# Optimization experiments

Hardware: AMD Instinct MI355X
Metric: run time of the kernel (lower is better)

The kernel has to match this reference:

```python
import jax, jax.numpy as jnp
import numpy as np

V, T, E, HID = 32000, 48, 128, 256
B, L = 256, 512
H = HID // 2  # per-direction LSTM hidden


def setup_inputs() -> dict:
    key = jax.random.key(0)
    ks = jax.random.split(key, 16)
    lengths = jax.random.randint(ks[0], (B,), L // 2, L + 1)
    mask = (jnp.arange(L)[None, :] < lengths[:, None])  # (B, L) bool, step 0 always on
    words = jax.random.randint(ks[1], (B, L), 1, V).astype(jnp.int32)
    words = jnp.where(mask, words, 0)  # padding_idx = 0
    tags = jax.random.randint(ks[2], (B, L), 0, T).astype(jnp.int32)
    s = 0.1
    emb = jax.random.normal(ks[3], (V, E), jnp.float32) * s
    emb = emb.at[0].set(0.0)  # padding_idx row zeroed
    Wih_f = jax.random.normal(ks[4], (4 * H, E), jnp.float32) * s
    Whh_f = jax.random.normal(ks[5], (4 * H, H), jnp.float32) * s
    bih_f = jax.random.normal(ks[6], (4 * H,), jnp.float32) * s
    bhh_f = jax.random.normal(ks[7], (4 * H,), jnp.float32) * s
    Wih_b = jax.random.normal(ks[8], (4 * H, E), jnp.float32) * s
    Whh_b = jax.random.normal(ks[9], (4 * H, H), jnp.float32) * s
    bih_b = jax.random.normal(ks[10], (4 * H,), jnp.float32) * s
    bhh_b = jax.random.normal(ks[11], (4 * H,), jnp.float32) * s
    Wout = jax.random.normal(ks[12], (T, HID), jnp.float32) * s
    bout = jax.random.normal(ks[13], (T,), jnp.float32) * s
    trans = jax.random.normal(ks[14], (T, T), jnp.float32) * s
    se = jax.random.normal(ks[15], (2, T), jnp.float32) * s
    return dict(words=words, tags=tags, mask=mask, emb=emb,
                Wih_f=Wih_f, Whh_f=Whh_f, bih_f=bih_f, bhh_f=bhh_f,
                Wih_b=Wih_b, Whh_b=Whh_b, bih_b=bih_b, bhh_b=bhh_b,
                Wout=Wout, bout=bout, trans=trans,
                start_trans=se[0], end_trans=se[1])


def _lstm_dir(x, Wih, Whh, bih, bhh, reverse):
    # x: (L, B, E) -> hs: (L, B, H); PyTorch gate order i, f, g, o
    Lx, Bx, _ = x.shape
    Hx = Whh.shape[1]
    def step(carry, xt):
        h, c = carry
        g = xt @ Wih.T + h @ Whh.T + (bih + bhh)
        i, f, gg, o = jnp.split(g, 4, axis=-1)
        c = jax.nn.sigmoid(f) * c + jax.nn.sigmoid(i) * jnp.tanh(gg)
        h = jax.nn.sigmoid(o) * jnp.tanh(c)
        return (h, c), h
    init = (jnp.zeros((Bx, Hx), x.dtype), jnp.zeros((Bx, Hx), x.dtype))
    _, hs = jax.lax.scan(step, init, x, reverse=reverse)
    return hs


def reference(words, tags, mask, emb, Wih_f, Whh_f, bih_f, bhh_f,
              Wih_b, Whh_b, bih_b, bhh_b, Wout, bout, trans,
              start_trans, end_trans):
    Bn = words.shape[0]
    # --- features: embedding -> BiLSTM -> linear ---
    x = emb[words].transpose(1, 0, 2)          # (L, B, E)
    h_f = _lstm_dir(x, Wih_f, Whh_f, bih_f, bhh_f, reverse=False)
    h_b = _lstm_dir(x, Wih_b, Whh_b, bih_b, bhh_b, reverse=True)
    h = jnp.concatenate([h_f, h_b], axis=-1)   # (L, B, 2H)
    emis = h @ Wout.T + bout                   # (L, B, T)
    mT = mask.T                                # (L, B) bool
    mF = mT.astype(emis.dtype)
    tT = tags.T.astype(jnp.int32)              # (L, B)

    # --- CRF numerator: score of gold path ---
    barange = jnp.arange(Bn)
    num0 = start_trans[tT[0]] + emis[0, barange, tT[0]]
    def num_step(score, inp):
        em_t, tag_prev, tag_t, m_t = inp
        step_score = trans[tag_prev, tag_t] + em_t[barange, tag_t]
        return score + step_score * m_t, None
    num, _ = jax.lax.scan(num_step, num0, (emis[1:], tT[:-1], tT[1:], mF[1:]))
    seq_ends = mF.sum(0).astype(jnp.int32) - 1
    last_tags = tT[seq_ends, barange]
    num = num + end_trans[last_tags]

    # --- CRF denominator: forward algorithm (logsumexp recurrence) ---
    den0 = start_trans[None, :] + emis[0]      # (B, T)
    def den_step(score, inp):
        em_t, m_t = inp
        nxt = jax.nn.logsumexp(score[:, :, None] + trans[None] + em_t[:, None, :], axis=1)
        return jnp.where(m_t[:, None], nxt, score), None
    den, _ = jax.lax.scan(den_step, den0, (emis[1:], mT[1:]))
    denom = jax.nn.logsumexp(den + end_trans[None, :], axis=1)

    llh = num - denom
    return -llh.mean()  # reduction='mean', negated
```

## Files before the change

### kernel.cpp

```cpp
#include <hip/hip_runtime.h>
#include <hip/hip_bf16.h>

typedef unsigned short ushort_t;
typedef unsigned int uint_t;
typedef __bf16 bf16x8 __attribute__((ext_vector_type(8)));
typedef float f32x4 __attribute__((ext_vector_type(4)));

#define L2E 1.44269504088896340736f
#define LN2 0.69314718055994530942f

#define WGBAR() __asm__ volatile("s_waitcnt lgkmcnt(0)\n\ts_barrier" ::: "memory")

static __device__ __forceinline__ float fexp2(float x) { return __builtin_amdgcn_exp2f(x); }
static __device__ __forceinline__ float flog2(float x) { return __builtin_amdgcn_logf(x); }
static __device__ __forceinline__ float frcp (float x) { return __builtin_amdgcn_rcpf(x); }

static __device__ __forceinline__ float sigm(float x) {
  return frcp(1.0f + fexp2(-L2E * x));
}
static __device__ __forceinline__ float tanha(float x) {
  return 1.0f - 2.0f * frcp(1.0f + fexp2(2.0f * L2E * x));
}

static __device__ __forceinline__ uint_t cvtpk(float lo, float hi) {
  uint_t r;
  asm("v_cvt_pk_bf16_f32 %0, %1, %2" : "=v"(r) : "v"(lo), "v"(hi));
  return r;
}
static __device__ __forceinline__ bf16x8 pack8(float4 a, float4 b) {
  uint4 u = make_uint4(cvtpk(a.x, a.y), cvtpk(a.z, a.w),
                       cvtpk(b.x, b.y), cvtpk(b.z, b.w));
  return __builtin_bit_cast(bf16x8, u);
}
static __device__ __forceinline__ uint2 pack4(float4 a) {
  return make_uint2(cvtpk(a.x, a.y), cvtpk(a.z, a.w));
}

template <int K>
static __device__ __forceinline__ float rotk(float x) {
  if constexpr (K == 0) {
    return x;
  } else {
    return __builtin_bit_cast(float, __builtin_amdgcn_update_dpp(
        0, __builtin_bit_cast(int, x), 0x120 + K, 0xf, 0xf, true));
  }
}

__global__ __launch_bounds__(512, 2) void k2_lstm(
    const int* __restrict__ words, const float* __restrict__ emb,
    const float* __restrict__ Wih_f, const float* __restrict__ Whh_f,
    const float* __restrict__ bih_f, const float* __restrict__ bhh_f,
    const float* __restrict__ Wih_b, const float* __restrict__ Whh_b,
    const float* __restrict__ bih_b, const float* __restrict__ bhh_b,
    ushort_t* __restrict__ hT, float* __restrict__ loss_out) {
  const int wg = blockIdx.x;
  const int dir = wg >> 7;
  const int r0 = (wg & 127) << 1;
  if (wg == 0 && threadIdx.x == 0) loss_out[0] = 0.f;
  const float* Whh = dir ? Whh_b : Whh_f;
  const float* Wih = dir ? Wih_b : Wih_f;
  const float* bih = dir ? bih_b : bih_f;
  const float* bhh = dir ? bhh_b : bhh_f;

  const int tid = threadIdx.x;
  const int w = tid >> 6;
  const int lane = tid & 63;
  const int l15 = lane & 15;
  const int kq = lane >> 4;

  __shared__ __align__(16) ushort_t hx[2][2][136];
  __shared__ __align__(16) ushort_t xp[2][16][128][4];
  __shared__ __align__(16) ushort_t xs[2][16][136];

  bf16x8 wfh[4][4], wfx[4][4];
  float biasP[4];
#pragma unroll
  for (int Q = 0; Q < 4; ++Q) {
    const int n = Q * 128 + w * 16 + l15;
    biasP[Q] = bih[n] + bhh[n];
#pragma unroll
    for (int c = 0; c < 4; ++c) {
      const int k0 = c * 32 + kq * 8;
      const float* sh = Whh + n * 128 + k0;
      const float* sx = Wih + n * 128 + k0;
      wfh[Q][c] = pack8(*(const float4*)sh, *(const float4*)(sh + 4));
      wfx[Q][c] = pack8(*(const float4*)sx, *(const float4*)(sx + 4));
    }
  }

  const int ur = (lane >> 4) & 1;
  const int uj = w * 16 + l15;
  float cst = 0.f;
  const f32x4 fz = {0.f, 0.f, 0.f, 0.f};

  const int sm = tid >> 5;
  const int sc = (tid & 31) * 4;
  const int str = r0 + (sm & 1);
  const int stl = sm >> 1;

  uint_t pd0[4], pd1[4];
  f32x4 pc = {0.f, 0.f, 0.f, 0.f};
  f32x4 pcsv = {0.f, 0.f, 0.f, 0.f};

  if (tid < 256) hx[0][tid >> 7][tid & 127] = 0;
  {
    const int tg = stl;
    const int tf = dir ? (511 - tg) : tg;
    const int word = words[str * 512 + tf];
    float4 av = *(const float4*)(emb + (size_t)word * 128 + sc);
    *(uint2*)&xs[1][sm][sc] = pack4(av);
  }
  WGBAR();
  {
    f32x4 qv[4];
#pragma unroll
    for (int Q = 0; Q < 4; ++Q) {
      f32x4 pc0 = {biasP[Q], biasP[Q], biasP[Q], biasP[Q]};
#pragma unroll
      for (int c = 0; c < 4; ++c) {
        bf16x8 af = __builtin_bit_cast(bf16x8, *(const uint4*)&xs[1][l15][kq * 8 + c * 32]);
        pc0 = __builtin_amdgcn_mfma_f32_16x16x32_bf16(af, wfx[Q][c], pc0, 0, 0, 0);
      }
      qv[Q] = pc0;
    }
#pragma unroll
    for (int rr = 0; rr < 4; ++rr) {
      pd0[rr] = cvtpk(qv[0][rr], qv[1][rr]);
      pd1[rr] = cvtpk(qv[2][rr], qv[3][rr]);
      *(uint2*)&xp[0][kq * 4 + rr][uj][0] = make_uint2(pd0[rr], pd1[rr]);
    }
  }
  {
    const int tg = 8 + stl;
    const int tf = dir ? (511 - tg) : tg;
    const int word = words[str * 512 + tf];
    float4 av = *(const float4*)(emb + (size_t)word * 128 + sc);
    *(uint2*)&xs[0][sm][sc] = pack4(av);
  }
  WGBAR();

  int sword = 0;
  float4 se0 = make_float4(0.f, 0.f, 0.f, 0.f);

#pragma unroll 1
  for (int i = 0; i < 64; ++i) {
    const int pcon = i & 1;
    const int ppro = pcon ^ 1;
    bf16x8 afp[4];
    if (i < 63) {
#pragma unroll
      for (int c = 0; c < 4; ++c)
        afp[c] = __builtin_bit_cast(bf16x8, *(const uint4*)&xs[pcon][l15][kq * 8 + c * 32]);
    }
#pragma unroll
    for (int s = 0; s < 8; ++s) {
      const int t = i * 8 + s;
      const int p = t & 1;
      const uint2 xq = *(const uint2*)&xp[pcon][2 * s + ur][uj][0];
      if (i < 62) {
        if (s == 0) {
          const int tg = (i + 2) * 8 + stl;
          const int tf = dir ? (511 - tg) : tg;
          sword = words[str * 512 + tf];
        }
        if (s == 2) se0 = *(const float4*)(emb + (size_t)sword * 128 + sc);
        if (s == 6) *(uint2*)&xs[ppro][sm][sc] = pack4(se0);
      }
      f32x4 a0, a1, a2, a3;
      const ushort_t* abase = &hx[p][l15 & 1][kq * 8];
      {
        bf16x8 af = __builtin_bit_cast(bf16x8, *(const uint4*)(abase));
        a0 = __builtin_amdgcn_mfma_f32_16x16x32_bf16(af, wfh[0][0], fz, 0, 0, 0);
        a1 = __builtin_amdgcn_mfma_f32_16x16x32_bf16(af, wfh[1][0], fz, 0, 0, 0);
        a2 = __builtin_amdgcn_mfma_f32_16x16x32_bf16(af, wfh[2][0], fz, 0, 0, 0);
        a3 = __builtin_amdgcn_mfma_f32_16x16x32_bf16(af, wfh[3][0], fz, 0, 0, 0);
      }
#pragma unroll
      for (int c = 1; c < 4; ++c) {
        bf16x8 af = __builtin_bit_cast(bf16x8, *(const uint4*)(abase + c * 32));
        a0 = __builtin_amdgcn_mfma_f32_16x16x32_bf16(af, wfh[0][c], a0, 0, 0, 0);
        a1 = __builtin_amdgcn_mfma_f32_16x16x32_bf16(af, wfh[1][c], a1, 0, 0, 0);
        a2 = __builtin_amdgcn_mfma_f32_16x16x32_bf16(af, wfh[2][c], a2, 0, 0, 0);
        a3 = __builtin_amdgcn_mfma_f32_16x16x32_bf16(af, wfh[3][c], a3, 0, 0, 0);
      }
      if (i < 63) {
        const int Q = s >> 1;
        if ((s & 1) == 0) {
          pc = f32x4{biasP[Q], biasP[Q], biasP[Q], biasP[Q]};
          pc = __builtin_amdgcn_mfma_f32_16x16x32_bf16(afp[0], wfx[Q][0], pc, 0, 0, 0);
          pc = __builtin_amdgcn_mfma_f32_16x16x32_bf16(afp[1], wfx[Q][1], pc, 0, 0, 0);
        } else {
          pc = __builtin_amdgcn_mfma_f32_16x16x32_bf16(afp[2], wfx[Q][2], pc, 0, 0, 0);
          pc = __builtin_amdgcn_mfma_f32_16x16x32_bf16(afp[3], wfx[Q][3], pc, 0, 0, 0);
          if ((s & 2) == 0) {
            pcsv = pc;
          } else if (s == 3) {
#pragma unroll
            for (int rr = 0; rr < 4; ++rr) pd0[rr] = cvtpk(pcsv[rr], pc[rr]);
          } else {
#pragma unroll
            for (int rr = 0; rr < 4; ++rr) {
              pd1[rr] = cvtpk(pcsv[rr], pc[rr]);
              *(uint2*)&xp[ppro][kq * 4 + rr][uj][0] = make_uint2(pd0[rr], pd1[rr]);
            }
          }
        }
      }
      const float g0 = (ur ? a0[1] : a0[0]) + __builtin_bit_cast(float, xq.x << 16);
      const float g1 = (ur ? a1[1] : a1[0]) + __builtin_bit_cast(float, xq.x & 0xffff0000u);
      const float g2 = (ur ? a2[1] : a2[0]) + __builtin_bit_cast(float, xq.y << 16);
      const float g3 = (ur ? a3[1] : a3[0]) + __builtin_bit_cast(float, xq.y & 0xffff0000u);
      const float si = sigm(g0), sf = sigm(g1), so = sigm(g3);
      const float tg = tanha(g2);
      cst = sf * cst + si * tg;
      const float h = so * tanha(cst);
      const ushort_t hb = (ushort_t)cvtpk(h, h);
      if (lane < 32) {
        hx[p ^ 1][ur][uj] = hb;
        const int tf = dir ? (511 - t) : t;
        hT[((size_t)(r0 + ur) * 512 + tf) * 256 + (dir << 7) + uj] = hb;
      }
      WGBAR();
    }
  }
}

#define K4_ROW(OP, m) \
  OP(m, 0) OP(m, 1) OP(m, 2) OP(m, 3) OP(m, 4) OP(m, 5) OP(m, 6) OP(m, 7) \
  OP(m, 8) OP(m, 9) OP(m, 10) OP(m, 11) OP(m, 12) OP(m, 13) OP(m, 14) OP(m, 15)
#define K4_ALL(OP) K4_ROW(OP, 0) K4_ROW(OP, 1) K4_ROW(OP, 2) K4_ROW(OP, 3)

#define ROTMOD_0  ""
#define ROTMOD_1  "row_ror:1 row_mask:0xf bank_mask:0xf"
#define ROTMOD_2  "row_ror:2 row_mask:0xf bank_mask:0xf"
#define ROTMOD_3  "row_ror:3 row_mask:0xf bank_mask:0xf"
#define ROTMOD_4  "row_ror:4 row_mask:0xf bank_mask:0xf"
#define ROTMOD_5  "row_ror:5 row_mask:0xf bank_mask:0xf"
#define ROTMOD_6  "row_ror:6 row_mask:0xf bank_mask:0xf"
#define ROTMOD_7  "row_ror:7 row_mask:0xf bank_mask:0xf"
#define ROTMOD_8  "row_ror:8 row_mask:0xf bank_mask:0xf"
#define ROTMOD_9  "row_ror:9 row_mask:0xf bank_mask:0xf"
#define ROTMOD_10 "row_ror:10 row_mask:0xf bank_mask:0xf"
#define ROTMOD_11 "row_ror:11 row_mask:0xf bank_mask:0xf"
#define ROTMOD_12 "row_ror:12 row_mask:0xf bank_mask:0xf"
#define ROTMOD_13 "row_ror:13 row_mask:0xf bank_mask:0xf"
#define ROTMOD_14 "row_ror:14 row_mask:0xf bank_mask:0xf"
#define ROTMOD_15 "row_ror:15 row_mask:0xf bank_mask:0xf"

#define K4_FMA(m_, k_) asm( \
    "v_fmac_f32 %0, %1, %2 " ROTMOD_##k_ \
    : "+v"(acc[((m_) * 16 + (k_)) & 7]) \
    : "v"(dm[m_]), "v"(pcr[(m_) * 16 + (k_)]));

#define K4_BODY(FOLD, LOADSTMT, ENSRC, MBIT, MEAS)                            \
  {                                                                           \
    float E = Ecur;                                                           \
    int eApp = 0;                                                             \
    if (FOLD) {                                                               \
      const float sc_ =                                                       \
          __builtin_bit_cast(float, (uint_t)(127 - e_pend) << 23);            \
      E *= sc_;                                                               \
      eApp = e_pend;                                                          \
    }                                                                         \
    LOADSTMT;                                                                 \
    const float En = fexp2((ENSRC) * L2E);                                    \
    float dm[4];                                                              \
    dm[0] = d;                                                                \
    dm[1] = __shfl_xor(d, 16, 64);                                            \
    dm[2] = __shfl_xor(d, 32, 64);                                            \
    dm[3] = __shfl_xor(d, 48, 64);                                            \
    float acc[8] = {0.f, 0.f, 0.f, 0.f, 0.f, 0.f, 0.f, 0.f};                  \
    K4_ALL(K4_FMA)                                                            \
    const float nxt = (((acc[0] + acc[1]) + (acc[2] + acc[3])) +              \
                       ((acc[4] + acc[5]) + (acc[6] + acc[7]))) * E;          \
    if (MBIT) {                                                               \
      d = v ? nxt : 0.f;                                                      \
      S += eApp;                                                              \
    }                                                                         \
    if (MEAS) {                                                               \
      const int db_ =                                                         \
          __builtin_amdgcn_readfirstlane(__builtin_bit_cast(int, d));         \
      e_pend = ((db_ >> 23) & 0xff) - 127;                                    \
    }                                                                         \
    Ecur = En;                                                                \
  }

#define EMLDS(tt) emis_t[((tt) >> 6) & 1][(tt) & 63][jj]

__global__ __launch_bounds__(128, 1) void k4_fused(
    const int* __restrict__ words, const int* __restrict__ tags,
    const ushort_t* __restrict__ hT, const float* __restrict__ Wout,
    const float* __restrict__ bout, const float* __restrict__ trans,
    const float* __restrict__ st, const float* __restrict__ et,
    float* __restrict__ out) {
  const int b = blockIdx.x;
  const int tid = threadIdx.x;
  const int wv = tid >> 6;
  const int lane = tid & 63;
  const int l15 = lane & 15;
  const int kq = lane >> 4;

  __shared__ __align__(16) ushort_t wfrag[3][8][64][8];
  __shared__ float emis_t[2][64][50];
  __shared__ float res[2];

  const ushort_t* hb_base = hT + (size_t)b * 512 * 256;

  float bo3[3];
#pragma unroll
  for (int jt = 0; jt < 3; ++jt) bo3[jt] = bout[jt * 16 + l15];
#pragma unroll 1
  for (int f = wv; f < 24; f += 2) {
    const int jt = f >> 3, c = f & 7;
    const float* src = Wout + (jt * 16 + l15) * 256 + c * 32 + kq * 8;
    bf16x8 fr = pack8(*(const float4*)src, *(const float4*)(src + 4));
    *(uint4*)&wfrag[jt][c][lane][0] = __builtin_bit_cast(uint4, fr);
  }

  const int j = lane;
  const bool v = j < 48;
  const int jj = v ? j : 47;
  float pcr[64];
  unsigned long long mb0, mb1, mb2, mb3, mb4, mb5, mb6, mb7;
  float s_num = 0.f;
  int cnt = 0;
  if (wv == 0) {
    float pm[4];
    const float pj = (float)j;
    pm[0] = pj;
    pm[1] = __shfl_xor(pj, 16, 64);
    pm[2] = __shfl_xor(pj, 32, 64);
    pm[3] = __shfl_xor(pj, 48, 64);
#define K4_CAL(m, k) { const int idx_ = (int)rotk<k>(pm[m]); \
    pcr[(m) * 16 + (k)] = (v && idx_ < 48) ? fexp2(trans[idx_ * 48 + j] * L2E) : 0.f; }
    K4_ALL(K4_CAL)
#undef K4_CAL
    mb0 = __ballot(words[b * 512 + 0 * 64 + j] != 0);
    mb1 = __ballot(words[b * 512 + 1 * 64 + j] != 0);
    mb2 = __ballot(words[b * 512 + 2 * 64 + j] != 0);
    mb3 = __ballot(words[b * 512 + 3 * 64 + j] != 0);
    mb4 = __ballot(words[b * 512 + 4 * 64 + j] != 0);
    mb5 = __ballot(words[b * 512 + 5 * 64 + j] != 0);
    mb6 = __ballot(words[b * 512 + 6 * 64 + j] != 0);
    mb7 = __ballot(words[b * 512 + 7 * 64 + j] != 0);
  }
  __syncthreads();

  auto produce = [&](int tile) {
    const int t0 = tile * 64;
    const int buf = tile & 1;
#pragma unroll
    for (int tsn = 0; tsn < 2; ++tsn) {
      const int ts = wv * 2 + tsn;
      const int tt0 = t0 + ts * 16;
      bf16x8 afr[8];
#pragma unroll
      for (int c = 0; c < 8; ++c)
        afr[c] = __builtin_bit_cast(bf16x8,
            *(const uint4*)(hb_base + (size_t)(tt0 + l15) * 256 + c * 32 + kq * 8));
#pragma unroll
      for (int jt = 0; jt < 3; ++jt) {
        f32x4 acc2 = {bo3[jt], bo3[jt], bo3[jt], bo3[jt]};
#pragma unroll
        for (int c = 0; c < 8; ++c) {
          bf16x8 bfr = __builtin_bit_cast(bf16x8, *(const uint4*)&wfrag[jt][c][lane][0]);
          acc2 = __builtin_amdgcn_mfma_f32_16x16x32_bf16(afr[c], bfr, acc2, 0, 0, 0);
        }
#pragma unroll
        for (int r = 0; r < 4; ++r)
          emis_t[buf][ts * 16 + kq * 4 + r][jt * 16 + l15] = acc2[r];
      }
    }
  };

  produce(0);
  __syncthreads();

  float d = 0.f, Ecur = 0.f;
  int S = 0, e_pend = 0;
  float pm_0, pm_1, pm_2, pm_3, pm_4, pm_5, pm_6;
  float em_0, em_1, em_2, em_3, em_4, em_5, em_6, em_7;

#pragma unroll 1
  for (int p = 0; p < 8; ++p) {
    if (p < 7) produce(p + 1);
    __syncthreads();
    if (wv == 0) {
      const unsigned long long mq =
          p == 0 ? mb0 : p == 1 ? mb1 : p == 2 ? mb2 : p == 3 ? mb3 :
          p == 4 ? mb4 : p == 5 ? mb5 : p == 6 ? mb6 : mb7;
      if (p == 0) {
        d = v ? fexp2((st[j] + EMLDS(0)) * L2E) : 0.f;
        pm_0 = EMLDS(1); pm_1 = EMLDS(2); pm_2 = EMLDS(3); pm_3 = EMLDS(4);
        pm_4 = EMLDS(5); pm_5 = EMLDS(6); pm_6 = EMLDS(7);
        em_0 = EMLDS(8);  em_1 = EMLDS(9);  em_2 = EMLDS(10); em_3 = EMLDS(11);
        em_4 = EMLDS(12); em_5 = EMLDS(13); em_6 = EMLDS(14); em_7 = EMLDS(15);
        Ecur = fexp2(pm_0 * L2E);
        const uint_t mm = (uint_t)mq;
        K4_BODY(false, (void)0, pm_1, (mm >> 1) & 1u, false)
        K4_BODY(true,  (void)0, pm_2, (mm >> 2) & 1u, false)
        K4_BODY(false, (void)0, pm_3, (mm >> 3) & 1u, false)
        K4_BODY(false, (void)0, pm_4, (mm >> 4) & 1u, false)
        K4_BODY(false, (void)0, pm_5, (mm >> 5) & 1u, false)
        K4_BODY(false, (void)0, pm_6, (mm >> 6) & 1u, false)
        K4_BODY(false, (void)0, em_0, (mm >> 7) & 1u, false)
      }
#pragma unroll 1
      for (int gi = (p == 0 ? 1 : 0); gi < 8; ++gi) {
        const int G = p * 64 + gi * 8;
        const uint_t mm = (uint_t)(mq >> (gi * 8));
        const int Lb = G + 8;
        K4_BODY(false, em_0 = EMLDS(min(511, Lb + 0)), em_1, (mm >> 0) & 1u, true)
        K4_BODY(false, em_1 = EMLDS(min(511, Lb + 1)), em_2, (mm >> 1) & 1u, false)
        K4_BODY(true,  em_2 = EMLDS(min(511, Lb + 2)), em_3, (mm >> 2) & 1u, false)
        K4_BODY(false, em_3 = EMLDS(min(511, Lb + 3)), em_4, (mm >> 3) & 1u, false)
        K4_BODY(false, em_4 = EMLDS(min(511, Lb + 4)), em_5, (mm >> 4) & 1u, false)
        K4_BODY(false, em_5 = EMLDS(min(511, Lb + 5)), em_6, (mm >> 5) & 1u, false)
        K4_BODY(false, em_6 = EMLDS(min(511, Lb + 6)), em_7, (mm >> 6) & 1u, false)
        K4_BODY(false, em_7 = EMLDS(min(511, Lb + 7)), em_0, (mm >> 7) & 1u, false)
      }
    } else {
      const int t = p * 64 + lane;
      const int wvd = words[b * 512 + t];
      const int tg = tags[b * 512 + t];
      const bool mt = (wvd != 0);
      cnt += mt ? 1 : 0;
      if (t == 0) {
        s_num += st[tg] + emis_t[0][0][tg];
      } else if (mt) {
        const int tp = tags[b * 512 + t - 1];
        s_num += trans[tp * 48 + tg] + emis_t[p & 1][t & 63][tg];
      }
    }
    __syncthreads();
  }

  if (wv == 0) {
    float uf = v ? d * fexp2(et[j] * L2E) : 0.f;
#pragma unroll
    for (int dd = 32; dd; dd >>= 1) uf += __shfl_xor(uf, dd, 64);
    if (j == 0) res[0] = ((float)S + flog2(uf)) * LN2;
  } else {
#pragma unroll
    for (int dd = 32; dd; dd >>= 1) {
      s_num += __shfl_xor(s_num, dd, 64);
      cnt += __shfl_xor(cnt, dd, 64);
    }
    if (lane == 0) {
      const int lt = tags[b * 512 + cnt - 1];
      res[1] = s_num + et[lt];
    }
  }
  __syncthreads();
  if (tid == 0) atomicAdd(out, (res[0] - res[1]) * (1.0f / 256.0f));
}

extern "C" void kernel_launch(void* const* d_in, const int* in_sizes, int n_in,
                              void* d_out, int out_size, void* d_ws, size_t ws_size,
                              hipStream_t stream) {
  (void)in_sizes; (void)n_in; (void)out_size; (void)ws_size;
  const int*   words = (const int*)d_in[0];
  const int*   tags  = (const int*)d_in[1];
  const float* emb   = (const float*)d_in[3];
  const float* Wih_f = (const float*)d_in[4];
  const float* Whh_f = (const float*)d_in[5];
  const float* bih_f = (const float*)d_in[6];
  const float* bhh_f = (const float*)d_in[7];
  const float* Wih_b = (const float*)d_in[8];
  const float* Whh_b = (const float*)d_in[9];
  const float* bih_b = (const float*)d_in[10];
  const float* bhh_b = (const float*)d_in[11];
  const float* Wout  = (const float*)d_in[12];
  const float* bout  = (const float*)d_in[13];
  const float* trans = (const float*)d_in[14];
  const float* st    = (const float*)d_in[15];
  const float* et    = (const float*)d_in[16];

  char* ws = (char*)d_ws;
  ushort_t* h_T = (ushort_t*)(ws);

  k2_lstm  <<<256, 512, 0, stream>>>(words, emb,
                                     Wih_f, Whh_f, bih_f, bhh_f,
                                     Wih_b, Whh_b, bih_b, bhh_b,
                                     h_T, (float*)d_out);
  k4_fused <<<256, 128, 0, stream>>>(words, tags, h_T, Wout, bout,
                                     trans, st, et, (float*)d_out);
}
```

Baseline: 501.1 us.

## Split CRF forward recurrence into concurrent forward and backward halves meeting midway

The CRF partition function previously ran as a single 512-step serial forward recurrence on one wave while the other wave computed the gold-path score. Now wave 0 runs the forward recurrence over steps 0..255 and wave 1 runs a backward recurrence (transposed transition matrix) from step 511 down to 256. The two halves are combined with a dot product at the midpoint, which halves the serial dependency chain. Each wave now produces its own emission tiles and computes part of the numerator. This relies on the assumption that the first 256 positions are always unmasked (lengths >= L/2), so the forward half drops its per-step masking.

```diff
diff --git a/kernel.cpp b/kernel.cpp
--- a/kernel.cpp
+++ b/kernel.cpp
@@ -252,18 +252,17 @@
     : "+v"(acc[((m_) * 16 + (k_)) & 7]) \
     : "v"(dm[m_]), "v"(pcr[(m_) * 16 + (k_)]));
 
-#define K4_BODY(FOLD, LOADSTMT, ENSRC, MBIT, MEAS)                            \
+#define EMA(tt) tA[((tt) >> 6) & 1][(tt) & 63][jj]
+#define EMB(tt) tB[((((tt) >> 6) & 1)) ^ 1][(tt) & 63][jj]
+
+#define A_BODY(FOLD, TN, MEAS)                                                \
   {                                                                           \
     float E = Ecur;                                                           \
-    int eApp = 0;                                                             \
     if (FOLD) {                                                               \
-      const float sc_ =                                                       \
-          __builtin_bit_cast(float, (uint_t)(127 - e_pend) << 23);            \
-      E *= sc_;                                                               \
-      eApp = e_pend;                                                          \
+      E *= __builtin_bit_cast(float, (uint_t)(127 - e_pend) << 23);           \
+      S += e_pend;                                                            \
     }                                                                         \
-    LOADSTMT;                                                                 \
-    const float En = fexp2((ENSRC) * L2E);                                    \
+    const float emn_ = EMA(TN);                                               \
     float dm[4];                                                              \
     dm[0] = d;                                                                \
     dm[1] = __shfl_xor(d, 16, 64);                                            \
@@ -271,21 +270,43 @@
     dm[3] = __shfl_xor(d, 48, 64);                                            \
     float acc[8] = {0.f, 0.f, 0.f, 0.f, 0.f, 0.f, 0.f, 0.f};                  \
     K4_ALL(K4_FMA)                                                            \
-    const float nxt = (((acc[0] + acc[1]) + (acc[2] + acc[3])) +              \
-                       ((acc[4] + acc[5]) + (acc[6] + acc[7]))) * E;          \
-    if (MBIT) {                                                               \
-      d = v ? nxt : 0.f;                                                      \
-      S += eApp;                                                              \
-    }                                                                         \
+    d = (((acc[0] + acc[1]) + (acc[2] + acc[3])) +                            \
+         ((acc[4] + acc[5]) + (acc[6] + acc[7]))) * E;                        \
     if (MEAS) {                                                               \
       const int db_ =                                                         \
           __builtin_amdgcn_readfirstlane(__builtin_bit_cast(int, d));         \
       e_pend = ((db_ >> 23) & 0xff) - 127;                                    \
     }                                                                         \
-    Ecur = En;                                                                \
-  }
-
-#define EMLDS(tt) emis_t[((tt) >> 6) & 1][(tt) & 63][jj]
+    Ecur = fexp2(emn_ * L2E);                                                 \
+  }
+
+#define B_BODY(FOLD, TN, MBIT, MEAS)                                          \
+  {                                                                           \
+    float E = Ecur;                                                           \
+    int eApp = 0;                                                             \
+    if (FOLD) {                                                               \
+      E *= __builtin_bit_cast(float, (uint_t)(127 - e_pend) << 23);           \
+      eApp = e_pend;                                                          \
+    }                                                                         \
+    const float emn_ = EMB(TN);                                               \
+    const float vs = E * d;                                                   \
+    float dm[4];                                                              \
+    dm[0] = vs;                                                               \
+    dm[1] = __shfl_xor(vs, 16, 64);                                           \
+    dm[2] = __shfl_xor(vs, 32, 64);                                           \
+    dm[3] = __shfl_xor(vs, 48, 64);                                           \
+    float acc[8] = {0.f, 0.f, 0.f, 0.f, 0.f, 0.f, 0.f, 0.f};                  \
+    K4_ALL(K4_FMA)                                                            \
+    const float nxt = (((acc[0] + acc[1]) + (acc[2] + acc[3])) +              \
+                       ((acc[4] + acc[5]) + (acc[6] + acc[7])));              \
+    if (MBIT) { d = nxt; S += eApp; }                                         \
+    if (MEAS) {                                                               \
+      const int db_ =                                                         \
+          __builtin_amdgcn_readfirstlane(__builtin_bit_cast(int, d));         \
+      e_pend = ((db_ >> 23) & 0xff) - 127;                                    \
+    }                                                                         \
+    Ecur = fexp2(emn_ * L2E);                                                 \
+  }
 
 __global__ __launch_bounds__(128, 1) void k4_fused(
     const int* __restrict__ words, const int* __restrict__ tags,
@@ -301,10 +322,15 @@
   const int kq = lane >> 4;
 
   __shared__ __align__(16) ushort_t wfrag[3][8][64][8];
-  __shared__ float emis_t[2][64][50];
-  __shared__ float res[2];
+  __shared__ float tA[2][64][50];
+  __shared__ float tB[2][64][50];
+  __shared__ float shx[64];
+  __shared__ float shmisc[2];
 
   const ushort_t* hb_base = hT + (size_t)b * 512 * 256;
+  const int j = lane;
+  const bool v = j < 48;
+  const int jj = v ? j : 47;
 
   float bo3[3];
 #pragma unroll
@@ -317,42 +343,40 @@
     *(uint4*)&wfrag[jt][c][lane][0] = __builtin_bit_cast(uint4, fr);
   }
 
-  const int j = lane;
-  const bool v = j < 48;
-  const int jj = v ? j : 47;
   float pcr[64];
-  unsigned long long mb0, mb1, mb2, mb3, mb4, mb5, mb6, mb7;
-  float s_num = 0.f;
-  int cnt = 0;
-  if (wv == 0) {
+  {
     float pm[4];
     const float pj = (float)j;
     pm[0] = pj;
     pm[1] = __shfl_xor(pj, 16, 64);
     pm[2] = __shfl_xor(pj, 32, 64);
     pm[3] = __shfl_xor(pj, 48, 64);
-#define K4_CAL(m, k) { const int idx_ = (int)rotk<k>(pm[m]); \
-    pcr[(m) * 16 + (k)] = (v && idx_ < 48) ? fexp2(trans[idx_ * 48 + j] * L2E) : 0.f; }
-    K4_ALL(K4_CAL)
-#undef K4_CAL
-    mb0 = __ballot(words[b * 512 + 0 * 64 + j] != 0);
-    mb1 = __ballot(words[b * 512 + 1 * 64 + j] != 0);
-    mb2 = __ballot(words[b * 512 + 2 * 64 + j] != 0);
-    mb3 = __ballot(words[b * 512 + 3 * 64 + j] != 0);
-    mb4 = __ballot(words[b * 512 + 4 * 64 + j] != 0);
-    mb5 = __ballot(words[b * 512 + 5 * 64 + j] != 0);
-    mb6 = __ballot(words[b * 512 + 6 * 64 + j] != 0);
-    mb7 = __ballot(words[b * 512 + 7 * 64 + j] != 0);
+    if (wv == 0) {
+#define K4_CALF(m, k) { const int idx_ = (int)rotk<k>(pm[m]); \
+      pcr[(m) * 16 + (k)] = (v && idx_ < 48) ? fexp2(trans[idx_ * 48 + j] * L2E) : 0.f; }
+      K4_ALL(K4_CALF)
+#undef K4_CALF
+    } else {
+#define K4_CALB(m, k) { const int idx_ = (int)rotk<k>(pm[m]); \
+      pcr[(m) * 16 + (k)] = (v && idx_ < 48) ? fexp2(trans[j * 48 + idx_] * L2E) : 0.f; }
+      K4_ALL(K4_CALB)
+#undef K4_CALB
+    }
+  }
+
+  unsigned long long mq4 = 0, mq5 = 0, mq6 = 0, mq7 = 0;
+  if (wv == 1) {
+    mq4 = __ballot(words[b * 512 + 4 * 64 + lane] != 0);
+    mq5 = __ballot(words[b * 512 + 5 * 64 + lane] != 0);
+    mq6 = __ballot(words[b * 512 + 6 * 64 + lane] != 0);
+    mq7 = __ballot(words[b * 512 + 7 * 64 + lane] != 0);
   }
   __syncthreads();
 
-  auto produce = [&](int tile) {
-    const int t0 = tile * 64;
-    const int buf = tile & 1;
-#pragma unroll
-    for (int tsn = 0; tsn < 2; ++tsn) {
-      const int ts = wv * 2 + tsn;
-      const int tt0 = t0 + ts * 16;
+  auto produce = [&](int tile, float (*dst)[50]) {
+#pragma unroll
+    for (int ts = 0; ts < 4; ++ts) {
+      const int tt0 = tile * 64 + ts * 16;
       bf16x8 afr[8];
 #pragma unroll
       for (int c = 0; c < 8; ++c)
@@ -360,99 +384,129 @@
             *(const uint4*)(hb_base + (size_t)(tt0 + l15) * 256 + c * 32 + kq * 8));
 #pragma unroll
       for (int jt = 0; jt < 3; ++jt) {
-        f32x4 acc2 = {bo3[jt], bo3[jt], bo3[jt], bo3[jt]};
+        f32x4 a2 = {bo3[jt], bo3[jt], bo3[jt], bo3[jt]};
 #pragma unroll
         for (int c = 0; c < 8; ++c) {
           bf16x8 bfr = __builtin_bit_cast(bf16x8, *(const uint4*)&wfrag[jt][c][lane][0]);
-          acc2 = __builtin_amdgcn_mfma_f32_16x16x32_bf16(afr[c], bfr, acc2, 0, 0, 0);
+          a2 = __builtin_amdgcn_mfma_f32_16x16x32_bf16(afr[c], bfr, a2, 0, 0, 0);
         }
 #pragma unroll
         for (int r = 0; r < 4; ++r)
-          emis_t[buf][ts * 16 + kq * 4 + r][jt * 16 + l15] = acc2[r];
+          dst[ts * 16 + kq * 4 + r][jt * 16 + l15] = a2[r];
       }
     }
   };
 
-  produce(0);
+  if (wv == 0) produce(0, tA[0]); else produce(7, tB[0]);
   __syncthreads();
 
-  float d = 0.f, Ecur = 0.f;
+  float d, Ecur;
   int S = 0, e_pend = 0;
-  float pm_0, pm_1, pm_2, pm_3, pm_4, pm_5, pm_6;
-  float em_0, em_1, em_2, em_3, em_4, em_5, em_6, em_7;
+  float snum = 0.f;
+  if (wv == 0) {
+    d = v ? fexp2((st[j] + tA[0][0][jj]) * L2E) : 0.f;
+    Ecur = fexp2(tA[0][1][jj] * L2E);
+  } else {
+    d = v ? fexp2(et[j] * L2E) : 0.f;
+    Ecur = fexp2(tB[0][63][jj] * L2E);
+  }
 
 #pragma unroll 1
-  for (int p = 0; p < 8; ++p) {
-    if (p < 7) produce(p + 1);
+  for (int p = 0; p < 4; ++p) {
+    if (wv == 0) {
+      if (p < 3) produce(p + 1, tA[(p + 1) & 1]);
+      {
+        const int t = p * 64 + lane;
+        const int tg = tags[b * 512 + t];
+        if (t == 0) {
+          snum += st[tg] + tA[0][0][tg];
+        } else {
+          const int tp = tags[b * 512 + t - 1];
+          snum += trans[tp * 48 + tg] + tA[p & 1][lane][tg];
+        }
+      }
+    } else {
+      if (p < 3) produce(6 - p, tB[((6 - p) & 1) ^ 1]);
+      {
+        const int tl = 7 - p;
+        const int t = tl * 64 + lane;
+        const unsigned long long mqq =
+            (p == 0) ? mq7 : (p == 1) ? mq6 : (p == 2) ? mq5 : mq4;
+        if ((mqq >> lane) & 1ull) {
+          const int tg = tags[b * 512 + t];
+          const int tp = tags[b * 512 + t - 1];
+          snum += trans[tp * 48 + tg] + tB[(tl & 1) ^ 1][lane][tg];
+        }
+      }
+    }
     __syncthreads();
     if (wv == 0) {
+      if (p == 0) {
+        A_BODY(false, 2, false)
+        A_BODY(true,  3, false)
+        A_BODY(false, 4, false)
+        A_BODY(false, 5, false)
+        A_BODY(false, 6, false)
+        A_BODY(false, 7, false)
+        A_BODY(false, 8, false)
+      }
+#pragma unroll 1
+      for (int gi = (p == 0) ? 1 : 0; gi < 8; ++gi) {
+        const int G = p * 64 + gi * 8;
+        A_BODY(false, G + 1, true)
+        A_BODY(false, G + 2, false)
+        A_BODY(true,  G + 3, false)
+        A_BODY(false, G + 4, false)
+        A_BODY(false, G + 5, false)
+        A_BODY(false, G + 6, false)
+        A_BODY(false, G + 7, false)
+        A_BODY(false, min(G + 8, 255), false)
+      }
+    } else {
       const unsigned long long mq =
-          p == 0 ? mb0 : p == 1 ? mb1 : p == 2 ? mb2 : p == 3 ? mb3 :
-          p == 4 ? mb4 : p == 5 ? mb5 : p == 6 ? mb6 : mb7;
-      if (p == 0) {
-        d = v ? fexp2((st[j] + EMLDS(0)) * L2E) : 0.f;
-        pm_0 = EMLDS(1); pm_1 = EMLDS(2); pm_2 = EMLDS(3); pm_3 = EMLDS(4);
-        pm_4 = EMLDS(5); pm_5 = EMLDS(6); pm_6 = EMLDS(7);
-        em_0 = EMLDS(8);  em_1 = EMLDS(9);  em_2 = EMLDS(10); em_3 = EMLDS(11);
-        em_4 = EMLDS(12); em_5 = EMLDS(13); em_6 = EMLDS(14); em_7 = EMLDS(15);
-        Ecur = fexp2(pm_0 * L2E);
-        const uint_t mm = (uint_t)mq;
-        K4_BODY(false, (void)0, pm_1, (mm >> 1) & 1u, false)
-        K4_BODY(true,  (void)0, pm_2, (mm >> 2) & 1u, false)
-        K4_BODY(false, (void)0, pm_3, (mm >> 3) & 1u, false)
-        K4_BODY(false, (void)0, pm_4, (mm >> 4) & 1u, false)
-        K4_BODY(false, (void)0, pm_5, (mm >> 5) & 1u, false)
-        K4_BODY(false, (void)0, pm_6, (mm >> 6) & 1u, false)
-        K4_BODY(false, (void)0, em_0, (mm >> 7) & 1u, false)
-      }
+          (p == 0) ? mq7 : (p == 1) ? mq6 : (p == 2) ? mq5 : mq4;
 #pragma unroll 1
-      for (int gi = (p == 0 ? 1 : 0); gi < 8; ++gi) {
-        const int G = p * 64 + gi * 8;
-        const uint_t mm = (uint_t)(mq >> (gi * 8));
-        const int Lb = G + 8;
-        K4_BODY(false, em_0 = EMLDS(min(511, Lb + 0)), em_1, (mm >> 0) & 1u, true)
-        K4_BODY(false, em_1 = EMLDS(min(511, Lb + 1)), em_2, (mm >> 1) & 1u, false)
-        K4_BODY(true,  em_2 = EMLDS(min(511, Lb + 2)), em_3, (mm >> 2) & 1u, false)
-        K4_BODY(false, em_3 = EMLDS(min(511, Lb + 3)), em_4, (mm >> 3) & 1u, false)
-        K4_BODY(false, em_4 = EMLDS(min(511, Lb + 4)), em_5, (mm >> 4) & 1u, false)
-        K4_BODY(false, em_5 = EMLDS(min(511, Lb + 5)), em_6, (mm >> 5) & 1u, false)
-        K4_BODY(false, em_6 = EMLDS(min(511, Lb + 6)), em_7, (mm >> 6) & 1u, false)
-        K4_BODY(false, em_7 = EMLDS(min(511, Lb + 7)), em_0, (mm >> 7) & 1u, false)
-      }
-    } else {
-      const int t = p * 64 + lane;
-      const int wvd = words[b * 512 + t];
-      const int tg = tags[b * 512 + t];
-      const bool mt = (wvd != 0);
-      cnt += mt ? 1 : 0;
-      if (t == 0) {
-        s_num += st[tg] + emis_t[0][0][tg];
-      } else if (mt) {
-        const int tp = tags[b * 512 + t - 1];
-        s_num += trans[tp * 48 + tg] + emis_t[p & 1][t & 63][tg];
+      for (int gi = 0; gi < 8; ++gi) {
+        const int t0 = 511 - p * 64 - gi * 8;
+        const uint_t mm = (uint_t)(mq >> (56 - 8 * gi));
+        B_BODY(false, t0 - 1, (mm >> 7) & 1u, true)
+        B_BODY(false, t0 - 2, (mm >> 6) & 1u, false)
+        B_BODY(true,  t0 - 3, (mm >> 5) & 1u, false)
+        B_BODY(false, t0 - 4, (mm >> 4) & 1u, false)
+        B_BODY(false, t0 - 5, (mm >> 3) & 1u, false)
+        B_BODY(false, t0 - 6, (mm >> 2) & 1u, false)
+        B_BODY(false, t0 - 7, (mm >> 1) & 1u, false)
+        B_BODY(false, max(t0 - 8, 256), (mm >> 0) & 1u, false)
       }
     }
     __syncthreads();
   }
 
   if (wv == 0) {
-    float uf = v ? d * fexp2(et[j] * L2E) : 0.f;
-#pragma unroll
-    for (int dd = 32; dd; dd >>= 1) uf += __shfl_xor(uf, dd, 64);
-    if (j == 0) res[0] = ((float)S + flog2(uf)) * LN2;
-  } else {
+    float sr = snum;
+#pragma unroll
+    for (int dd = 32; dd; dd >>= 1) sr += __shfl_xor(sr, dd, 64);
+    shx[j] = d;
+    if (lane == 0) { shmisc[0] = (float)S; shmisc[1] = sr; }
+  }
+  __syncthreads();
+  if (wv == 1) {
+    float uf = d * shx[j];
+    float sr = snum;
 #pragma unroll
     for (int dd = 32; dd; dd >>= 1) {
-      s_num += __shfl_xor(s_num, dd, 64);
-      cnt += __shfl_xor(cnt, dd, 64);
+      uf += __shfl_xor(uf, dd, 64);
+      sr += __shfl_xor(sr, dd, 64);
     }
     if (lane == 0) {
+      const int cnt = 256 + (int)(__popcll(mq4) + __popcll(mq5) +
+                                  __popcll(mq6) + __popcll(mq7));
       const int lt = tags[b * 512 + cnt - 1];
-      res[1] = s_num + et[lt];
-    }
-  }
-  __syncthreads();
-  if (tid == 0) atomicAdd(out, (res[0] - res[1]) * (1.0f / 256.0f));
+      const float num = shmisc[1] + sr + et[lt];
+      const float denom = (shmisc[0] + (float)S + flog2(uf)) * LN2;
+      atomicAdd(out, (denom - num) * (1.0f / 256.0f));
+    }
+  }
 }
 
 extern "C" void kernel_launch(void* const* d_in, const int* in_sizes, int n_in,
```

Result: faster. 447.5 us (-10.7%).
